# Optimization experiments

Measured on AMD Instinct MI355X. Metric: run time of the kernel, lower is better.

## Reference

```python
import jax, jax.numpy as jnp
import numpy as np

N_NODES = 200000
D = 128            # in_channels
B_GRAPHS = 512     # batch_size
STEPS = 3          # processing_steps


def setup_inputs() -> dict:
    key = jax.random.key(0)
    k = jax.random.split(key, 6)
    x = jax.random.normal(k[0], (N_NODES, D), dtype=jnp.float32)
    batch = jnp.sort(jax.random.randint(k[1], (N_NODES,), 0, B_GRAPHS, dtype=jnp.int64))
    s = 0.1
    W_ih = jax.random.normal(k[2], (3 * D, 2 * D), dtype=jnp.float32) * s
    W_hh = jax.random.normal(k[3], (3 * D, D), dtype=jnp.float32) * s
    b_ih = jax.random.normal(k[4], (3 * D,), dtype=jnp.float32) * s
    b_hh = jax.random.normal(k[5], (3 * D,), dtype=jnp.float32) * s
    return {"x": x, "batch": batch, "batch_size": B_GRAPHS,
            "W_ih": W_ih, "W_hh": W_hh, "b_ih": b_ih, "b_hh": b_hh}


def _gru_cell(inp, h, W_ih, W_hh, b_ih, b_hh):
    # inp: [B, 2d], h: [B, d]; PyTorch GRU gate order: r, z, n
    gi = inp @ W_ih.T + b_ih  # [B, 3d]
    gh = h @ W_hh.T + b_hh    # [B, 3d]
    gi_r, gi_z, gi_n = jnp.split(gi, 3, axis=-1)
    gh_r, gh_z, gh_n = jnp.split(gh, 3, axis=-1)
    r = jax.nn.sigmoid(gi_r + gh_r)
    z = jax.nn.sigmoid(gi_z + gh_z)
    n = jnp.tanh(gi_n + r * gh_n)
    return (1.0 - z) * n + z * h


def reference(x, batch, batch_size, W_ih, W_hh, b_ih, b_hh):
    B = batch_size
    d = x.shape[1]
    h = jnp.zeros((B, d), dtype=x.dtype)
    q_star = jnp.zeros((B, 2 * d), dtype=x.dtype)
    for _ in range(STEPS):
        h = _gru_cell(q_star, h, W_ih, W_hh, b_ih, b_hh)
        q = h  # num_layers=1: output == new hidden state
        e = jnp.sum(x * q[batch], axis=-1)  # [N]
        m = jax.ops.segment_max(e, batch, num_segments=B)
        ex = jnp.exp(e - m[batch])
        s = jax.ops.segment_sum(ex, batch, num_segments=B)
        a = ex / (s[batch] + 1e-16)  # segment softmax weights [N]
        r = jax.ops.segment_sum(a[:, None] * x, batch, num_segments=B)  # [B, d]
        q_star = jnp.concatenate([q, r], axis=-1)
    return q_star
```

## Files before the change

kernel.cpp:

```cpp
#include <hip/hip_runtime.h>
#include <math.h>

constexpr int D = 128;
constexpr int B = 512;
constexpr int STEPS = 3;
constexpr int NW_IH = 3 * D * 2 * D;
constexpr int NW_HH = 3 * D * D;

__device__ __forceinline__ float sigmoidf_(float x) { return 1.f / (1.f + __expf(-x)); }
__device__ __forceinline__ float bflo(unsigned int u) { return __uint_as_float(u << 16); }
__device__ __forceinline__ float bfhi(unsigned int u) { return __uint_as_float(u & 0xffff0000u); }
__device__ __forceinline__ unsigned short f2bf_rn(float f) {
    unsigned int u = __float_as_uint(f);
    u += 0x7fffu + ((u >> 16) & 1u);
    return (unsigned short)(u >> 16);
}

__global__ __launch_bounds__(256) void k_prep(const float* __restrict__ Wih,
        const float* __restrict__ Whh, const int* __restrict__ batch, int n,
        unsigned short* __restrict__ wih_bf, unsigned short* __restrict__ whh_bf,
        int* __restrict__ seg) {
    int i = blockIdx.x * blockDim.x + threadIdx.x;
    if (i < NW_IH) wih_bf[i] = f2bf_rn(Wih[i]);
    else if (i < NW_IH + NW_HH) whh_bf[i - NW_IH] = f2bf_rn(Whh[i - NW_IH]);
    if (i <= B) {
        int lo = 0, hi = n;
        while (lo < hi) { int mid = (lo + hi) >> 1; if (batch[mid] < i) lo = mid + 1; else hi = mid; }
        seg[i] = lo;
    }
}

__global__ __launch_bounds__(1024, 8) void k_set2set(
        const float* __restrict__ x,
        const unsigned short* __restrict__ wih_bf,
        const unsigned short* __restrict__ whh_bf,
        const float* __restrict__ bih, const float* __restrict__ bhh,
        const int* __restrict__ seg, float* __restrict__ out) {
    __shared__ float s_q[2 * D];
    __shared__ float s_h[D];
    __shared__ float s_gi[3 * D], s_gh[3 * D];
    __shared__ float sm[32], sl[32];
    __shared__ float s_M, s_inv;
    __shared__ float rpart[16][D];

    const int b = blockIdx.x;
    const int tid = threadIdx.x;
    const int start = seg[b], end = seg[b + 1];
    const int lane32 = tid & 31;
    const int hw = tid >> 5;

    if (tid < 2 * D) s_q[tid] = 0.f;
    if (tid < D) s_h[tid] = 0.f;
    __syncthreads();

    for (int step = 0; step < STEPS; ++step) {
        if (tid < 3 * D) {
            const int t = tid;
            float gi = bih[t], gh = bhh[t];
            const uint4* wr = (const uint4*)(wih_bf + (size_t)t * (2 * D));
#pragma unroll 2
            for (int c = 0; c < (2 * D) / 8; ++c) {
                uint4 w = wr[c];
                const float* q = &s_q[c * 8];
                gi = fmaf(bflo(w.x), q[0], gi); gi = fmaf(bfhi(w.x), q[1], gi);
                gi = fmaf(bflo(w.y), q[2], gi); gi = fmaf(bfhi(w.y), q[3], gi);
                gi = fmaf(bflo(w.z), q[4], gi); gi = fmaf(bfhi(w.z), q[5], gi);
                gi = fmaf(bflo(w.w), q[6], gi); gi = fmaf(bfhi(w.w), q[7], gi);
            }
            const uint4* vr = (const uint4*)(whh_bf + (size_t)t * D);
#pragma unroll 2
            for (int c = 0; c < D / 8; ++c) {
                uint4 w = vr[c];
                const float* hh = &s_h[c * 8];
                gh = fmaf(bflo(w.x), hh[0], gh); gh = fmaf(bfhi(w.x), hh[1], gh);
                gh = fmaf(bflo(w.y), hh[2], gh); gh = fmaf(bfhi(w.y), hh[3], gh);
                gh = fmaf(bflo(w.z), hh[4], gh); gh = fmaf(bfhi(w.z), hh[5], gh);
                gh = fmaf(bflo(w.w), hh[6], gh); gh = fmaf(bfhi(w.w), hh[7], gh);
            }
            s_gi[t] = gi; s_gh[t] = gh;
        }
        __syncthreads();
        if (tid < D) {
            const int t = tid;
            float r  = sigmoidf_(s_gi[t] + s_gh[t]);
            float z  = sigmoidf_(s_gi[D + t] + s_gh[D + t]);
            float nn = tanhf(s_gi[2 * D + t] + r * s_gh[2 * D + t]);
            float hn = (1.f - z) * nn + z * s_h[t];
            s_h[t] = hn;
            s_q[t] = hn;
        }
        __syncthreads();

        const float4 qf = *(const float4*)&s_h[lane32 * 4];
        float m_run = -INFINITY, l_run = 0.f;
        float4 acc = {0.f, 0.f, 0.f, 0.f};
        for (int node = start + hw; node < end; node += 32) {
            float4 xv = ((const float4*)(x + (size_t)node * D))[lane32];
            float p = fmaf(xv.x, qf.x, fmaf(xv.y, qf.y, fmaf(xv.z, qf.z, xv.w * qf.w)));
            p += __shfl_xor(p, 16, 64);
            p += __shfl_xor(p, 8, 64);
            p += __shfl_xor(p, 4, 64);
            p += __shfl_xor(p, 2, 64);
            p += __shfl_xor(p, 1, 64);
            float nm = fmaxf(m_run, p);
            float scale = __expf(m_run - nm);
            float a = __expf(p - nm);
            l_run = fmaf(l_run, scale, a);
            acc.x = fmaf(acc.x, scale, a * xv.x);
            acc.y = fmaf(acc.y, scale, a * xv.y);
            acc.z = fmaf(acc.z, scale, a * xv.z);
            acc.w = fmaf(acc.w, scale, a * xv.w);
            m_run = nm;
        }
        if (lane32 == 0) { sm[hw] = m_run; sl[hw] = l_run; }
        __syncthreads();
        if (tid == 0) {
            float M = -INFINITY;
            for (int i = 0; i < 32; ++i) M = fmaxf(M, sm[i]);
            float L = 0.f;
            for (int i = 0; i < 32; ++i)
                L += (sm[i] == -INFINITY) ? 0.f : sl[i] * __expf(sm[i] - M);
            s_M = M;
            s_inv = 1.f / (L + 1e-16f);
        }
        __syncthreads();
        const float fac = (m_run == -INFINITY) ? 0.f : __expf(m_run - s_M);
        acc.x *= fac; acc.y *= fac; acc.z *= fac; acc.w *= fac;
        acc.x += __shfl_down(acc.x, 32, 64);
        acc.y += __shfl_down(acc.y, 32, 64);
        acc.z += __shfl_down(acc.z, 32, 64);
        acc.w += __shfl_down(acc.w, 32, 64);
        const int wave = tid >> 6;
        const int lane64 = tid & 63;
        if (lane64 < 32) ((float4*)rpart[wave])[lane64] = acc;
        __syncthreads();
        if (tid < D) {
            float v = 0.f;
#pragma unroll
            for (int w = 0; w < 16; ++w) v += rpart[w][tid];
            s_q[D + tid] = v * s_inv;
        }
        __syncthreads();
    }

    if (tid < 2 * D) out[(size_t)b * (2 * D) + tid] = s_q[tid];
}

extern "C" void kernel_launch(void* const* d_in, const int* in_sizes, int n_in,
                              void* d_out, int out_size, void* d_ws, size_t ws_size,
                              hipStream_t stream) {
    const float* x    = (const float*)d_in[0];
    const int*   batch= (const int*)d_in[1];
    const float* Wih  = (const float*)d_in[3];
    const float* Whh  = (const float*)d_in[4];
    const float* bih  = (const float*)d_in[5];
    const float* bhh  = (const float*)d_in[6];
    const int n = in_sizes[0] / D;

    char* ws = (char*)d_ws;
    int* seg = (int*)ws;
    unsigned short* wih_bf = (unsigned short*)(ws + 4096);
    unsigned short* whh_bf = (unsigned short*)(ws + 4096 + (size_t)NW_IH * 2);

    const int total = NW_IH + NW_HH;
    k_prep<<<(total + 255) / 256, 256, 0, stream>>>(Wih, Whh, batch, n, wih_bf, whh_bf, seg);
    k_set2set<<<B, 1024, 0, stream>>>(x, wih_bf, whh_bf, bih, bhh, seg, (float*)d_out);
}
```

Before: 252.5 us.

## Split GRU rows across thread pairs and use 16-lane node groups with 2-node unroll

The GRU matvec now uses 768 threads, with two threads per output row each covering half the reduction, combined by a shuffle. Shared-memory operands are read as float4. The attention pass now gives each node to 16 lanes holding 8 floats each, so 64 nodes are in flight per iteration, and the loop processes two nodes per trip to overlap loads. The single-thread merge of softmax partials is replaced by a wave-level shuffle reduction that every wave computes redundantly, which removes one barrier. The cost is more registers per thread and redundant reduction work.

```diff
diff --git a/kernel.cpp b/kernel.cpp
--- a/kernel.cpp
+++ b/kernel.cpp
@@ -36,48 +36,55 @@
         const unsigned short* __restrict__ whh_bf,
         const float* __restrict__ bih, const float* __restrict__ bhh,
         const int* __restrict__ seg, float* __restrict__ out) {
-    __shared__ float s_q[2 * D];
-    __shared__ float s_h[D];
+    __shared__ __align__(16) float s_q[2 * D];
+    __shared__ __align__(16) float s_h[D];
     __shared__ float s_gi[3 * D], s_gh[3 * D];
-    __shared__ float sm[32], sl[32];
-    __shared__ float s_M, s_inv;
-    __shared__ float rpart[16][D];
+    __shared__ float sm[64], sl[64];
+    __shared__ __align__(16) float rpart[16][D];
 
     const int b = blockIdx.x;
     const int tid = threadIdx.x;
     const int start = seg[b], end = seg[b + 1];
-    const int lane32 = tid & 31;
-    const int hw = tid >> 5;
+    const int g = tid >> 4;
+    const int s = tid & 15;
 
     if (tid < 2 * D) s_q[tid] = 0.f;
     if (tid < D) s_h[tid] = 0.f;
     __syncthreads();
 
     for (int step = 0; step < STEPS; ++step) {
-        if (tid < 3 * D) {
-            const int t = tid;
-            float gi = bih[t], gh = bhh[t];
-            const uint4* wr = (const uint4*)(wih_bf + (size_t)t * (2 * D));
-#pragma unroll 2
-            for (int c = 0; c < (2 * D) / 8; ++c) {
+        if (tid < 768) {
+            const int row  = tid >> 1;
+            const int half = tid & 1;
+            float gi = half ? 0.f : bih[row];
+            float gh = half ? bhh[row] : 0.f;
+            const float4* q4 = (const float4*)s_q;
+            const float4* h4 = (const float4*)s_h;
+            const uint4* wr = (const uint4*)(wih_bf + (size_t)row * (2 * D)) + half * 16;
+#pragma unroll 4
+            for (int c = 0; c < 16; ++c) {
                 uint4 w = wr[c];
-                const float* q = &s_q[c * 8];
-                gi = fmaf(bflo(w.x), q[0], gi); gi = fmaf(bfhi(w.x), q[1], gi);
-                gi = fmaf(bflo(w.y), q[2], gi); gi = fmaf(bfhi(w.y), q[3], gi);
-                gi = fmaf(bflo(w.z), q[4], gi); gi = fmaf(bfhi(w.z), q[5], gi);
-                gi = fmaf(bflo(w.w), q[6], gi); gi = fmaf(bfhi(w.w), q[7], gi);
+                float4 qa = q4[half * 32 + c * 2];
+                float4 qb = q4[half * 32 + c * 2 + 1];
+                gi = fmaf(bflo(w.x), qa.x, gi); gi = fmaf(bfhi(w.x), qa.y, gi);
+                gi = fmaf(bflo(w.y), qa.z, gi); gi = fmaf(bfhi(w.y), qa.w, gi);
+                gi = fmaf(bflo(w.z), qb.x, gi); gi = fmaf(bfhi(w.z), qb.y, gi);
+                gi = fmaf(bflo(w.w), qb.z, gi); gi = fmaf(bfhi(w.w), qb.w, gi);
             }
-            const uint4* vr = (const uint4*)(whh_bf + (size_t)t * D);
-#pragma unroll 2
-            for (int c = 0; c < D / 8; ++c) {
+            const uint4* vr = (const uint4*)(whh_bf + (size_t)row * D) + half * 8;
+#pragma unroll 4
+            for (int c = 0; c < 8; ++c) {
                 uint4 w = vr[c];
-                const float* hh = &s_h[c * 8];
-                gh = fmaf(bflo(w.x), hh[0], gh); gh = fmaf(bfhi(w.x), hh[1], gh);
-                gh = fmaf(bflo(w.y), hh[2], gh); gh = fmaf(bfhi(w.y), hh[3], gh);
-                gh = fmaf(bflo(w.z), hh[4], gh); gh = fmaf(bfhi(w.z), hh[5], gh);
-                gh = fmaf(bflo(w.w), hh[6], gh); gh = fmaf(bfhi(w.w), hh[7], gh);
+                float4 ha = h4[half * 16 + c * 2];
+                float4 hb = h4[half * 16 + c * 2 + 1];
+                gh = fmaf(bflo(w.x), ha.x, gh); gh = fmaf(bfhi(w.x), ha.y, gh);
+                gh = fmaf(bflo(w.y), ha.z, gh); gh = fmaf(bfhi(w.y), ha.w, gh);
+                gh = fmaf(bflo(w.z), hb.x, gh); gh = fmaf(bfhi(w.z), hb.y, gh);
+                gh = fmaf(bflo(w.w), hb.z, gh); gh = fmaf(bfhi(w.w), hb.w, gh);
             }
-            s_gi[t] = gi; s_gh[t] = gh;
+            gi += __shfl_xor(gi, 1, 64);
+            gh += __shfl_xor(gh, 1, 64);
+            if (!half) { s_gi[row] = gi; s_gh[row] = gh; }
         }
         __syncthreads();
         if (tid < D) {
@@ -91,54 +98,98 @@
         }
         __syncthreads();
 
-        const float4 qf = *(const float4*)&s_h[lane32 * 4];
+        const float4 q0 = ((const float4*)s_h)[s * 2];
+        const float4 q1 = ((const float4*)s_h)[s * 2 + 1];
         float m_run = -INFINITY, l_run = 0.f;
-        float4 acc = {0.f, 0.f, 0.f, 0.f};
-        for (int node = start + hw; node < end; node += 32) {
-            float4 xv = ((const float4*)(x + (size_t)node * D))[lane32];
-            float p = fmaf(xv.x, qf.x, fmaf(xv.y, qf.y, fmaf(xv.z, qf.z, xv.w * qf.w)));
-            p += __shfl_xor(p, 16, 64);
+        float4 acc0 = {0.f, 0.f, 0.f, 0.f};
+        float4 acc1 = {0.f, 0.f, 0.f, 0.f};
+
+        auto process = [&](const float4& v0, const float4& v1) {
+            float p;
+            p = v0.x * q0.x;
+            p = fmaf(v0.y, q0.y, p); p = fmaf(v0.z, q0.z, p); p = fmaf(v0.w, q0.w, p);
+            p = fmaf(v1.x, q1.x, p); p = fmaf(v1.y, q1.y, p);
+            p = fmaf(v1.z, q1.z, p); p = fmaf(v1.w, q1.w, p);
+            p += __shfl_xor(p, 1, 64);
+            p += __shfl_xor(p, 2, 64);
+            p += __shfl_xor(p, 4, 64);
             p += __shfl_xor(p, 8, 64);
-            p += __shfl_xor(p, 4, 64);
-            p += __shfl_xor(p, 2, 64);
-            p += __shfl_xor(p, 1, 64);
             float nm = fmaxf(m_run, p);
-            float scale = __expf(m_run - nm);
-            float a = __expf(p - nm);
-            l_run = fmaf(l_run, scale, a);
-            acc.x = fmaf(acc.x, scale, a * xv.x);
-            acc.y = fmaf(acc.y, scale, a * xv.y);
-            acc.z = fmaf(acc.z, scale, a * xv.z);
-            acc.w = fmaf(acc.w, scale, a * xv.w);
+            float sc = __expf(m_run - nm);
+            float a  = __expf(p - nm);
+            l_run = fmaf(l_run, sc, a);
+            acc0.x = fmaf(acc0.x, sc, a * v0.x);
+            acc0.y = fmaf(acc0.y, sc, a * v0.y);
+            acc0.z = fmaf(acc0.z, sc, a * v0.z);
+            acc0.w = fmaf(acc0.w, sc, a * v0.w);
+            acc1.x = fmaf(acc1.x, sc, a * v1.x);
+            acc1.y = fmaf(acc1.y, sc, a * v1.y);
+            acc1.z = fmaf(acc1.z, sc, a * v1.z);
+            acc1.w = fmaf(acc1.w, sc, a * v1.w);
             m_run = nm;
-        }
-        if (lane32 == 0) { sm[hw] = m_run; sl[hw] = l_run; }
-        __syncthreads();
-        if (tid == 0) {
-            float M = -INFINITY;
-            for (int i = 0; i < 32; ++i) M = fmaxf(M, sm[i]);
-            float L = 0.f;
-            for (int i = 0; i < 32; ++i)
-                L += (sm[i] == -INFINITY) ? 0.f : sl[i] * __expf(sm[i] - M);
-            s_M = M;
-            s_inv = 1.f / (L + 1e-16f);
-        }
-        __syncthreads();
-        const float fac = (m_run == -INFINITY) ? 0.f : __expf(m_run - s_M);
-        acc.x *= fac; acc.y *= fac; acc.z *= fac; acc.w *= fac;
-        acc.x += __shfl_down(acc.x, 32, 64);
-        acc.y += __shfl_down(acc.y, 32, 64);
-        acc.z += __shfl_down(acc.z, 32, 64);
-        acc.w += __shfl_down(acc.w, 32, 64);
-        const int wave = tid >> 6;
-        const int lane64 = tid & 63;
-        if (lane64 < 32) ((float4*)rpart[wave])[lane64] = acc;
+        };
+
+        for (int n0 = start + g; n0 < end; n0 += 128) {
+            const int n1 = n0 + 64;
+            const float* p0 = x + (size_t)n0 * D + s * 8;
+            float4 a0 = *(const float4*)p0;
+            float4 a1 = *(const float4*)(p0 + 4);
+            if (n1 < end) {
+                const float* p1 = x + (size_t)n1 * D + s * 8;
+                float4 b0 = *(const float4*)p1;
+                float4 b1 = *(const float4*)(p1 + 4);
+                process(a0, a1);
+                process(b0, b1);
+            } else {
+                process(a0, a1);
+            }
+        }
+
+        if (s == 0) { sm[g] = m_run; sl[g] = l_run; }
+        __syncthreads();
+
+        {
+            const float mv = sm[tid & 63];
+            const float lv = sl[tid & 63];
+            float M = mv;
+            M = fmaxf(M, __shfl_xor(M, 1, 64));
+            M = fmaxf(M, __shfl_xor(M, 2, 64));
+            M = fmaxf(M, __shfl_xor(M, 4, 64));
+            M = fmaxf(M, __shfl_xor(M, 8, 64));
+            M = fmaxf(M, __shfl_xor(M, 16, 64));
+            M = fmaxf(M, __shfl_xor(M, 32, 64));
+            float term = (mv == -INFINITY) ? 0.f : lv * __expf(mv - M);
+            term += __shfl_xor(term, 1, 64);
+            term += __shfl_xor(term, 2, 64);
+            term += __shfl_xor(term, 4, 64);
+            term += __shfl_xor(term, 8, 64);
+            term += __shfl_xor(term, 16, 64);
+            term += __shfl_xor(term, 32, 64);
+            const float inv = 1.f / (term + 1e-16f);
+            const float fac = (m_run == -INFINITY) ? 0.f : __expf(m_run - M) * inv;
+            acc0.x *= fac; acc0.y *= fac; acc0.z *= fac; acc0.w *= fac;
+            acc1.x *= fac; acc1.y *= fac; acc1.z *= fac; acc1.w *= fac;
+        }
+        acc0.x += __shfl_xor(acc0.x, 16, 64); acc0.y += __shfl_xor(acc0.y, 16, 64);
+        acc0.z += __shfl_xor(acc0.z, 16, 64); acc0.w += __shfl_xor(acc0.w, 16, 64);
+        acc1.x += __shfl_xor(acc1.x, 16, 64); acc1.y += __shfl_xor(acc1.y, 16, 64);
+        acc1.z += __shfl_xor(acc1.z, 16, 64); acc1.w += __shfl_xor(acc1.w, 16, 64);
+        acc0.x += __shfl_xor(acc0.x, 32, 64); acc0.y += __shfl_xor(acc0.y, 32, 64);
+        acc0.z += __shfl_xor(acc0.z, 32, 64); acc0.w += __shfl_xor(acc0.w, 32, 64);
+        acc1.x += __shfl_xor(acc1.x, 32, 64); acc1.y += __shfl_xor(acc1.y, 32, 64);
+        acc1.z += __shfl_xor(acc1.z, 32, 64); acc1.w += __shfl_xor(acc1.w, 32, 64);
+
+        const int wv = tid >> 6;
+        if ((tid & 63) < 16) {
+            float4* dst = (float4*)&rpart[wv][s * 8];
+            dst[0] = acc0; dst[1] = acc1;
+        }
         __syncthreads();
         if (tid < D) {
             float v = 0.f;
 #pragma unroll
             for (int w = 0; w < 16; ++w) v += rpart[w][tid];
-            s_q[D + tid] = v * s_inv;
+            s_q[D + tid] = v;
         }
         __syncthreads();
     }
```

After: 259.5 us. +2.8%, slower.
